# Performance work log

Measured on AMD Instinct MI355X. Metric: run time of the kernel, lower is better.

The kernel has to match this reference:

```python
import jax, jax.numpy as jnp
import numpy as np

HEADS = 8
DIM_HEAD = 64
LN_EPS = 1e-5


def rotate_half(x):
    # pairs (x0,x1) -> (-x1,x0), interleaved layout (einops '(d r)' with r=2)
    x1 = x[..., 0::2]
    x2 = x[..., 1::2]
    return jnp.stack((-x2, x1), axis=-1).reshape(x.shape)


def apply_rope(freqs, x):
    return x * jnp.cos(freqs) + rotate_half(x) * jnp.sin(freqs)


def setup_inputs() -> dict:
    key = jax.random.key(0)
    ks = jax.random.split(key, 4)
    b, n, dim = 2, 4096, 512
    inner = HEADS * DIM_HEAD
    x = jax.random.normal(ks[0], (b, n, dim), dtype=jnp.float32)
    rotary_time_emb = jax.random.uniform(ks[1], (b, n, DIM_HEAD), jnp.float32, 0.0, 6.283185)
    ln_w = jnp.ones((dim,), jnp.float32)
    ln_b = jnp.zeros((dim,), jnp.float32)
    w_qkv = jax.random.normal(ks[2], (inner * 3, dim), jnp.float32) * (dim ** -0.5)
    w_out = jax.random.normal(ks[3], (dim, inner), jnp.float32) * (inner ** -0.5)
    b_out = jnp.zeros((dim,), jnp.float32)
    return dict(x=x, rotary_time_emb=rotary_time_emb, ln_w=ln_w, ln_b=ln_b,
                w_qkv=w_qkv, w_out=w_out, b_out=b_out)


def reference(x, rotary_time_emb, ln_w, ln_b, w_qkv, w_out, b_out):
    b, n, dim = x.shape
    # LayerNorm
    mu = jnp.mean(x, axis=-1, keepdims=True)
    var = jnp.var(x, axis=-1, keepdims=True)
    xn = (x - mu) * jax.lax.rsqrt(var + LN_EPS) * ln_w + ln_b
    # QKV projection (Linear, no bias)
    qkv = xn @ w_qkv.T  # [b, n, 3*inner]
    q, k, v = jnp.split(qkv, 3, axis=-1)

    def to_heads(t):
        return t.reshape(b, n, HEADS, DIM_HEAD).transpose(0, 2, 1, 3)  # b h n d

    q, k, v = to_heads(q), to_heads(k), to_heads(v)
    freqs = rotary_time_emb[:, None, :, :]  # b 1 n d, broadcast over heads
    q = apply_rope(freqs, q)
    k = apply_rope(freqs, k)
    v = apply_rope(freqs, v)  # rotate_value=True
    scale = jnp.asarray(DIM_HEAD ** -0.5, dtype=x.dtype)
    scores = jnp.einsum('bhqd,bhkd->bhqk', q, k) * scale
    attn = jax.nn.softmax(scores, axis=-1)
    out = jnp.einsum('bhqk,bhkd->bhqd', attn, v)
    out = apply_rope(-freqs, out)  # inverse rotation of the output
    out = out.transpose(0, 2, 1, 3).reshape(b, n, HEADS * DIM_HEAD)
    return out @ w_out.T + b_out
```

## Files before the change

kernel.cpp:

```cpp
#include <hip/hip_runtime.h>
#include <cmath>

typedef short bf16x8 __attribute__((ext_vector_type(8)));
typedef float f32x2 __attribute__((ext_vector_type(2)));
typedef float f32x4 __attribute__((ext_vector_type(4)));
typedef float f32x16 __attribute__((ext_vector_type(16)));

#define NSEQ 4096
#define BATCH 2
#define DIM 512
#define HEADS 8
#define NROWS (BATCH * NSEQ)
#define QKVN (3 * DIM)

__device__ __forceinline__ unsigned short f2bf(float f) {
  unsigned int u = __float_as_uint(f);
  u += 0x7fffu + ((u >> 16) & 1u);
  return (unsigned short)(u >> 16);
}
__device__ __forceinline__ float bf2f(unsigned short h) {
  return __uint_as_float(((unsigned int)h) << 16);
}
__device__ __forceinline__ void gload16(const unsigned short* g, unsigned short* l) {
  __builtin_amdgcn_global_load_lds((const __attribute__((address_space(1))) unsigned int*)g,
                                   (__attribute__((address_space(3))) unsigned int*)l, 16, 0, 0);
}

__global__ __launch_bounds__(256) void k_tables(const float* __restrict__ rot,
                                                float* __restrict__ cosT,
                                                float* __restrict__ sinT) {
  int i = blockIdx.x * 256 + threadIdx.x;
  float f = rot[i];
  cosT[i] = cosf(f);
  sinT[i] = sinf(f);
}

__global__ __launch_bounds__(256) void k_cvt(const float* __restrict__ src,
                                             unsigned short* __restrict__ dst, int n) {
  int i = blockIdx.x * 256 + threadIdx.x;
  if (i < n) dst[i] = f2bf(src[i]);
}

__global__ __launch_bounds__(256) void k_ln(const float* __restrict__ x,
                                            const float* __restrict__ w,
                                            const float* __restrict__ bb,
                                            unsigned short* __restrict__ xn) {
  int row = blockIdx.x * 4 + (threadIdx.x >> 6);
  int lane = threadIdx.x & 63;
  const float* xr = x + (size_t)row * DIM;
  float v[8];
  float s = 0.f;
#pragma unroll
  for (int j = 0; j < 8; ++j) { v[j] = xr[lane + j * 64]; s += v[j]; }
#pragma unroll
  for (int m = 1; m < 64; m <<= 1) s += __shfl_xor(s, m);
  float mu = s * (1.0f / DIM);
  float q = 0.f;
#pragma unroll
  for (int j = 0; j < 8; ++j) { float d = v[j] - mu; q += d * d; }
#pragma unroll
  for (int m = 1; m < 64; m <<= 1) q += __shfl_xor(q, m);
  float rs = rsqrtf(q * (1.0f / DIM) + 1e-5f);
#pragma unroll
  for (int j = 0; j < 8; ++j) {
    int col = lane + j * 64;
    xn[(size_t)row * DIM + col] = f2bf((v[j] - mu) * rs * w[col] + bb[col]);
  }
}

template <int EPI>
__global__ __launch_bounds__(256) void k_gemm(const unsigned short* __restrict__ A,
                                              const unsigned short* __restrict__ B,
                                              void* __restrict__ C,
                                              const float* __restrict__ bias,
                                              int M, int N, int K) {
  __shared__ __align__(16) unsigned short As[2][128 * 32];
  __shared__ __align__(16) unsigned short Bs[2][128 * 32];
  int bm = blockIdx.x, bn = blockIdx.y;
  int tid = threadIdx.x;
  int lane = tid & 63, w = tid >> 6;
  int wm = (w >> 1) << 6, wn = (w & 1) << 6;
  f32x4 acc[4][4] = {};

#define GSTAGE(KT, BUF) do { \
  _Pragma("unroll") \
  for (int i = 0; i < 2; ++i) { \
    int c = tid + (i << 8); \
    int row = c >> 2, kc = (c & 3) << 3; \
    gload16(A + (size_t)(bm * 128 + row) * K + (KT) + kc, &As[BUF][(w * 64 + i * 256) * 8]); \
    gload16(B + (size_t)(bn * 128 + row) * K + (KT) + kc, &Bs[BUF][(w * 64 + i * 256) * 8]); \
  } } while (0)

  GSTAGE(0, 0);
  __syncthreads();
  int nk = K >> 5;
  for (int t = 0; t < nk; ++t) {
    int cur = t & 1;
    if (t + 1 < nk) GSTAGE((t + 1) << 5, cur ^ 1);
    bf16x8 af[4], bfr[4];
#pragma unroll
    for (int mi = 0; mi < 4; ++mi)
      af[mi] = *(const bf16x8*)&As[cur][(wm + mi * 16 + (lane & 15)) * 32 + ((lane >> 4) << 3)];
#pragma unroll
    for (int ni = 0; ni < 4; ++ni)
      bfr[ni] = *(const bf16x8*)&Bs[cur][(wn + ni * 16 + (lane & 15)) * 32 + ((lane >> 4) << 3)];
#pragma unroll
    for (int mi = 0; mi < 4; ++mi)
#pragma unroll
      for (int ni = 0; ni < 4; ++ni)
        acc[mi][ni] = __builtin_amdgcn_mfma_f32_16x16x32_bf16(af[mi], bfr[ni], acc[mi][ni], 0, 0, 0);
    __syncthreads();
  }
#undef GSTAGE
#pragma unroll
  for (int mi = 0; mi < 4; ++mi) {
#pragma unroll
    for (int ni = 0; ni < 4; ++ni) {
#pragma unroll
      for (int r = 0; r < 4; ++r) {
        int gm = bm * 128 + wm + mi * 16 + ((lane >> 4) << 2) + r;
        int gn = bn * 128 + wn + ni * 16 + (lane & 15);
        if (EPI == 0) {
          ((unsigned short*)C)[(size_t)gm * N + gn] = f2bf(acc[mi][ni][r]);
        } else {
          ((float*)C)[(size_t)gm * N + gn] = acc[mi][ni][r] + bias[gn];
        }
      }
    }
  }
}

__global__ __launch_bounds__(256) void k_rope_split(const unsigned short* __restrict__ qkv,
                                                    const float* __restrict__ cosT,
                                                    const float* __restrict__ sinT,
                                                    unsigned short* __restrict__ qh,
                                                    unsigned short* __restrict__ kh,
                                                    unsigned short* __restrict__ vt) {
  __shared__ unsigned short vs[128][65];
  const float QSC = 0.125f * 1.44269504f;
  int nt = blockIdx.x, bh = blockIdx.y;
  int b = bh >> 3, h = bh & 7;
  int n0 = nt * 128;
  int t = threadIdx.x;
  int sub = t >> 3, cc = t & 7;
#pragma unroll
  for (int rr = 0; rr < 4; ++rr) {
    int row = rr * 32 + sub;
    int n = n0 + row;
    size_t base = ((size_t)(b * NSEQ + n)) * QKVN + h * 64 + cc * 8;
    const float* cb = cosT + ((size_t)(b * NSEQ + n)) * 64 + cc * 8;
    const float* sb = sinT + ((size_t)(b * NSEQ + n)) * 64 + cc * 8;
    float c[8], sn[8];
#pragma unroll
    for (int j = 0; j < 8; ++j) { c[j] = cb[j]; sn[j] = sb[j]; }
    bf16x8 qv = *(const bf16x8*)(qkv + base);
    bf16x8 kv = *(const bf16x8*)(qkv + base + 512);
    bf16x8 vv = *(const bf16x8*)(qkv + base + 1024);
    union { bf16x8 v; unsigned short u[8]; } yq, yk;
#pragma unroll
    for (int j = 0; j < 8; j += 2) {
      {
        float e = bf2f((unsigned short)qv[j]), o = bf2f((unsigned short)qv[j + 1]);
        yq.u[j]     = f2bf((e * c[j] - o * sn[j]) * QSC);
        yq.u[j + 1] = f2bf((o * c[j + 1] + e * sn[j + 1]) * QSC);
      }
      {
        float e = bf2f((unsigned short)kv[j]), o = bf2f((unsigned short)kv[j + 1]);
        yk.u[j]     = f2bf(e * c[j] - o * sn[j]);
        yk.u[j + 1] = f2bf(o * c[j + 1] + e * sn[j + 1]);
      }
      {
        float e = bf2f((unsigned short)vv[j]), o = bf2f((unsigned short)vv[j + 1]);
        vs[row][cc * 8 + j]     = f2bf(e * c[j] - o * sn[j]);
        vs[row][cc * 8 + j + 1] = f2bf(o * c[j + 1] + e * sn[j + 1]);
      }
    }
    *(bf16x8*)(qh + ((size_t)bh * NSEQ + n) * 64 + cc * 8) = yq.v;
    *(bf16x8*)(kh + ((size_t)bh * NSEQ + n) * 64 + cc * 8) = yk.v;
  }
  __syncthreads();
  int d = t >> 2, c4 = t & 3;
#pragma unroll
  for (int g = 0; g < 4; ++g) {
    union { bf16x8 v; unsigned short u[8]; } tv;
#pragma unroll
    for (int j = 0; j < 8; ++j) tv.u[j] = vs[c4 * 32 + g * 8 + j][d];
    *(bf16x8*)(vt + ((size_t)bh * 64 + d) * NSEQ + n0 + c4 * 32 + g * 8) = tv.v;
  }
}

__global__ __launch_bounds__(256, 2) void k_attn(const unsigned short* __restrict__ Qh,
                                                 const unsigned short* __restrict__ Kh,
                                                 const unsigned short* __restrict__ VT,
                                                 float* __restrict__ opart,
                                                 float* __restrict__ lpart) {
  __shared__ __align__(16) unsigned short Ks[2][64 * 64];
  __shared__ __align__(16) unsigned short Vs[2][64 * 64];
  int bid = blockIdx.x;
  int bh   = (bid & 7) + 8 * ((bid >> 7) & 1);
  int qt   = (bid >> 3) & 15;
  int half = (bid >> 8) & 1;
  int tid = threadIdx.x;
  int w = tid >> 6, lane = tid & 63;
  int lq = lane & 31, hi = lane >> 5;
  int q0 = qt * 256 + w * 64;
  int kv0 = half * 2048;

  const unsigned short* Kbh = Kh + (size_t)bh * NSEQ * 64;
  const unsigned short* Vbh = VT + (size_t)bh * 64 * NSEQ;

  const unsigned short* QbA = Qh + ((size_t)bh * NSEQ + q0 + lq) * 64 + hi * 8;
  const unsigned short* QbB = QbA + 32 * 64;
  bf16x8 qfA[4], qfB[4];
#pragma unroll
  for (int j = 0; j < 4; ++j) {
    qfA[j] = *(const bf16x8*)(QbA + j * 16);
    qfB[j] = *(const bf16x8*)(QbB + j * 16);
  }

  int c0 = w * 64 + lane;
  int r0 = c0 >> 3, sw0 = ((c0 & 7) ^ (r0 & 7)) << 3;
  int c1 = c0 + 256;
  int r1 = c1 >> 3, sw1 = ((c1 & 7) ^ (r1 & 7)) << 3;
  int ld0 = (w * 64) * 8, ld1 = (256 + w * 64) * 8;

  f32x16 accA0 = (f32x16)0.0f, accA1 = (f32x16)0.0f;
  f32x16 accB0 = (f32x16)0.0f, accB1 = (f32x16)0.0f;
  float lA = 0.f, lB = 0.f;
  int swz = (lq & 7) << 4;

  gload16(Kbh + ((size_t)kv0 + r0) * 64 + sw0, &Ks[0][ld0]);
  gload16(Kbh + ((size_t)kv0 + r1) * 64 + sw1, &Ks[0][ld1]);
  gload16(Vbh + (size_t)r0 * NSEQ + kv0 + sw0, &Vs[0][ld0]);
  gload16(Vbh + (size_t)r1 * NSEQ + kv0 + sw1, &Vs[0][ld1]);
  __syncthreads();

  for (int t = 0; t < 32; ++t) {
    int cur = t & 1;
    if (t < 31) {
      int tg = kv0 + (t + 1) * 64;
      gload16(Kbh + ((size_t)tg + r0) * 64 + sw0, &Ks[cur ^ 1][ld0]);
      gload16(Kbh + ((size_t)tg + r1) * 64 + sw1, &Ks[cur ^ 1][ld1]);
      gload16(Vbh + (size_t)r0 * NSEQ + tg + sw0, &Vs[cur ^ 1][ld0]);
      gload16(Vbh + (size_t)r1 * NSEQ + tg + sw1, &Vs[cur ^ 1][ld1]);
    }
    const char* kb_ = (const char*)&Ks[cur][0];
    const char* vb_ = (const char*)&Vs[cur][0];
#pragma unroll
    for (int ph = 0; ph < 2; ++ph) {
      f32x16 sA = (f32x16)0.0f, sB = (f32x16)0.0f;
      __builtin_amdgcn_s_setprio(1);
#pragma unroll
      for (int j = 0; j < 4; ++j) {
        int cb = j * 32 + hi * 16;
        bf16x8 a = *(const bf16x8*)(kb_ + (ph * 32 + lq) * 128 + (cb ^ swz));
        sA = __builtin_amdgcn_mfma_f32_32x32x16_bf16(a, qfA[j], sA, 0, 0, 0);
        sB = __builtin_amdgcn_mfma_f32_32x32x16_bf16(a, qfB[j], sB, 0, 0, 0);
      }
      __builtin_amdgcn_s_setprio(0);
#pragma unroll
      for (int r = 0; r < 16; ++r) sA[r] = __builtin_amdgcn_exp2f(sA[r]);
#pragma unroll
      for (int r = 0; r < 16; ++r) sB[r] = __builtin_amdgcn_exp2f(sB[r]);
      {
        union { f32x16 v; f32x2 p[8]; } ua, ub; ua.v = sA; ub.v = sB;
        f32x2 a01 = ua.p[0] + ua.p[1], a23 = ua.p[2] + ua.p[3];
        f32x2 a45 = ua.p[4] + ua.p[5], a67 = ua.p[6] + ua.p[7];
        f32x2 ta = (a01 + a23) + (a45 + a67);
        lA += ta.x + ta.y;
        f32x2 b01 = ub.p[0] + ub.p[1], b23 = ub.p[2] + ub.p[3];
        f32x2 b45 = ub.p[4] + ub.p[5], b67 = ub.p[6] + ub.p[7];
        f32x2 tb = (b01 + b23) + (b45 + b67);
        lB += tb.x + tb.y;
      }
      unsigned int dwA[8], dwB[8];
#pragma unroll
      for (int m = 0; m < 8; ++m) {
        asm("v_cvt_pk_bf16_f32 %0, %1, %2" : "=v"(dwA[m]) : "v"(sA[2 * m]), "v"(sA[2 * m + 1]));
        asm("v_cvt_pk_bf16_f32 %0, %1, %2" : "=v"(dwB[m]) : "v"(sB[2 * m]), "v"(sB[2 * m + 1]));
      }
      __builtin_amdgcn_s_setprio(1);
#pragma unroll
      for (int kk = 0; kk < 2; ++kk) {
        const int B = 4 * kk;
        unsigned int svA0 = hi ? dwA[B + 0] : dwA[B + 2];
        unsigned int svA1 = hi ? dwA[B + 1] : dwA[B + 3];
        unsigned int svB0 = hi ? dwB[B + 0] : dwB[B + 2];
        unsigned int svB1 = hi ? dwB[B + 1] : dwB[B + 3];
        unsigned int rvA0 = (unsigned int)__shfl_xor((int)svA0, 32);
        unsigned int rvA1 = (unsigned int)__shfl_xor((int)svA1, 32);
        unsigned int rvB0 = (unsigned int)__shfl_xor((int)svB0, 32);
        unsigned int rvB1 = (unsigned int)__shfl_xor((int)svB1, 32);
        union { unsigned int d[4]; bf16x8 v; } puA, puB;
        puA.d[0] = hi ? rvA0 : dwA[B + 0];
        puA.d[1] = hi ? rvA1 : dwA[B + 1];
        puA.d[2] = hi ? dwA[B + 2] : rvA0;
        puA.d[3] = hi ? dwA[B + 3] : rvA1;
        puB.d[0] = hi ? rvB0 : dwB[B + 0];
        puB.d[1] = hi ? rvB1 : dwB[B + 1];
        puB.d[2] = hi ? dwB[B + 2] : rvB0;
        puB.d[3] = hi ? dwB[B + 3] : rvB1;
        int cb = (ph * 2 + kk) * 32 + hi * 16;
        bf16x8 v0 = *(const bf16x8*)(vb_ + lq * 128 + (cb ^ swz));
        bf16x8 v1 = *(const bf16x8*)(vb_ + (32 + lq) * 128 + (cb ^ swz));
        accA0 = __builtin_amdgcn_mfma_f32_32x32x16_bf16(v0, puA.v, accA0, 0, 0, 0);
        accA1 = __builtin_amdgcn_mfma_f32_32x32x16_bf16(v1, puA.v, accA1, 0, 0, 0);
        accB0 = __builtin_amdgcn_mfma_f32_32x32x16_bf16(v0, puB.v, accB0, 0, 0, 0);
        accB1 = __builtin_amdgcn_mfma_f32_32x32x16_bf16(v1, puB.v, accB1, 0, 0, 0);
      }
      __builtin_amdgcn_s_setprio(0);
    }
    __syncthreads();
  }

  float lsumA = lA + __shfl_xor(lA, 32);
  float lsumB = lB + __shfl_xor(lB, 32);
  size_t qrowA = (size_t)(half * 16 + bh) * NSEQ + q0 + lq;
  size_t qrowB = qrowA + 32;
  if (hi == 0) {
    lpart[qrowA] = lsumA;
    lpart[qrowB] = lsumB;
  }
  float* obA = opart + qrowA * 64;
  float* obB = opart + qrowB * 64;
#pragma unroll
  for (int rg = 0; rg < 4; ++rg) {
    float4 a0 = make_float4(accA0[4 * rg + 0], accA0[4 * rg + 1], accA0[4 * rg + 2], accA0[4 * rg + 3]);
    float4 a1 = make_float4(accA1[4 * rg + 0], accA1[4 * rg + 1], accA1[4 * rg + 2], accA1[4 * rg + 3]);
    float4 b0 = make_float4(accB0[4 * rg + 0], accB0[4 * rg + 1], accB0[4 * rg + 2], accB0[4 * rg + 3]);
    float4 b1 = make_float4(accB1[4 * rg + 0], accB1[4 * rg + 1], accB1[4 * rg + 2], accB1[4 * rg + 3]);
    *(float4*)(obA + 8 * rg + 4 * hi) = a0;
    *(float4*)(obA + 32 + 8 * rg + 4 * hi) = a1;
    *(float4*)(obB + 8 * rg + 4 * hi) = b0;
    *(float4*)(obB + 32 + 8 * rg + 4 * hi) = b1;
  }
}

__global__ __launch_bounds__(256) void k_combine(const float* __restrict__ opart,
                                                 const float* __restrict__ lpart,
                                                 const float* __restrict__ cosT,
                                                 const float* __restrict__ sinT,
                                                 unsigned short* __restrict__ ao) {
  int bh = blockIdx.y;
  int b = bh >> 3, h = bh & 7;
  int t = threadIdx.x;
  int q = blockIdx.x * 16 + (t >> 4);
  int d = (t & 15) * 4;
  size_t i0 = (size_t)bh * NSEQ + q;
  const size_t HOFF = (size_t)16 * NSEQ;
  float4 o0 = *(const float4*)(opart + i0 * 64 + d);
  float4 o1 = *(const float4*)(opart + (i0 + HOFF) * 64 + d);
  float inv = 1.0f / (lpart[i0] + lpart[i0 + HOFF]);
  float4 c4 = *(const float4*)(cosT + ((size_t)b * NSEQ + q) * 64 + d);
  float4 s4 = *(const float4*)(sinT + ((size_t)b * NSEQ + q) * 64 + d);
  float yx = (o0.x + o1.x) * inv;
  float yy = (o0.y + o1.y) * inv;
  float yz = (o0.z + o1.z) * inv;
  float yw = (o0.w + o1.w) * inv;
  float r0 = yx * c4.x + yy * s4.x;
  float r1 = yy * c4.y - yx * s4.y;
  float r2 = yz * c4.z + yw * s4.z;
  float r3 = yw * c4.w - yz * s4.w;
  unsigned int w0, w1;
  asm("v_cvt_pk_bf16_f32 %0, %1, %2" : "=v"(w0) : "v"(r0), "v"(r1));
  asm("v_cvt_pk_bf16_f32 %0, %1, %2" : "=v"(w1) : "v"(r2), "v"(r3));
  unsigned int uu[2] = {w0, w1};
  *(uint2*)(ao + ((size_t)b * NSEQ + q) * DIM + h * 64 + d) = *(uint2*)uu;
}

extern "C" void kernel_launch(void* const* d_in, const int* in_sizes, int n_in,
                              void* d_out, int out_size, void* d_ws, size_t ws_size,
                              hipStream_t stream) {
  const float* x    = (const float*)d_in[0];
  const float* rot  = (const float*)d_in[1];
  const float* lnw  = (const float*)d_in[2];
  const float* lnb  = (const float*)d_in[3];
  const float* wqkv = (const float*)d_in[4];
  const float* wout = (const float*)d_in[5];
  const float* bout = (const float*)d_in[6];
  float* out = (float*)d_out;

  char* ws = (char*)d_ws;
  const size_t MB = (size_t)1 << 20;
  float* cosT          = (float*)(ws + 0 * MB);
  float* sinT          = (float*)(ws + 2 * MB);
  unsigned short* wqkb = (unsigned short*)(ws + 4 * MB);
  float* lpart         = (float*)(ws + 5 * MB + 512 * 1024);
  unsigned short* wob  = (unsigned short*)(ws + 6 * MB);
  unsigned short* xn   = (unsigned short*)(ws + 8 * MB);
  float* opart         = (float*)(ws + 8 * MB);
  unsigned short* qkv  = (unsigned short*)(ws + 16 * MB);
  unsigned short* qh   = (unsigned short*)(ws + 40 * MB);
  unsigned short* ao   = (unsigned short*)(ws + 40 * MB);
  unsigned short* kh   = (unsigned short*)(ws + 48 * MB);
  unsigned short* vt   = (unsigned short*)(ws + 56 * MB);

  k_tables<<<(BATCH * NSEQ * 64) / 256, 256, 0, stream>>>(rot, cosT, sinT);
  k_cvt<<<(QKVN * DIM + 255) / 256, 256, 0, stream>>>(wqkv, wqkb, QKVN * DIM);
  k_cvt<<<(DIM * DIM + 255) / 256, 256, 0, stream>>>(wout, wob, DIM * DIM);
  k_ln<<<NROWS / 4, 256, 0, stream>>>(x, lnw, lnb, xn);
  k_gemm<0><<<dim3(NROWS / 128, QKVN / 128), 256, 0, stream>>>(xn, wqkb, qkv, nullptr,
                                                               NROWS, QKVN, DIM);
  k_rope_split<<<dim3(NSEQ / 128, 16), 256, 0, stream>>>(qkv, cosT, sinT, qh, kh, vt);
  k_attn<<<512, 256, 0, stream>>>(qh, kh, vt, opart, lpart);
  k_combine<<<dim3(NSEQ / 16, 16), 256, 0, stream>>>(opart, lpart, cosT, sinT, ao);
  k_gemm<1><<<dim3(NROWS / 128, DIM / 128), 256, 0, stream>>>(ao, wob, out, bout,
                                                              NROWS, DIM, DIM);
}
```

Baseline: 148.1 us.

## Split attention KV range into four parts and store partial outputs as bf16

Attention now splits the key/value sequence into four 1024-long chunks instead of two, doubling the grid to 1024 blocks and raising the launch-bounds occupancy hint to 4 blocks per CU. The aim is better load balance and latency hiding across the 256 CUs. Partial outputs are written as bf16 instead of fp32, so the workspace traffic stays about the same despite twice as many partials. The combine kernel sums four partials, which adds bf16 rounding error to the unnormalised accumulators. lpart moves to avoid overlapping the larger buffer.

Result: slower. 581.5 us (+292.6%).

```diff
diff --git a/kernel.cpp b/kernel.cpp
--- a/kernel.cpp
+++ b/kernel.cpp
@@ -189,22 +189,22 @@
   }
 }
 
-__global__ __launch_bounds__(256, 2) void k_attn(const unsigned short* __restrict__ Qh,
+__global__ __launch_bounds__(256, 4) void k_attn(const unsigned short* __restrict__ Qh,
                                                  const unsigned short* __restrict__ Kh,
                                                  const unsigned short* __restrict__ VT,
-                                                 float* __restrict__ opart,
+                                                 unsigned short* __restrict__ opart,
                                                  float* __restrict__ lpart) {
   __shared__ __align__(16) unsigned short Ks[2][64 * 64];
   __shared__ __align__(16) unsigned short Vs[2][64 * 64];
   int bid = blockIdx.x;
   int bh   = (bid & 7) + 8 * ((bid >> 7) & 1);
   int qt   = (bid >> 3) & 15;
-  int half = (bid >> 8) & 1;
+  int quarter = (bid >> 8) & 3;
   int tid = threadIdx.x;
   int w = tid >> 6, lane = tid & 63;
   int lq = lane & 31, hi = lane >> 5;
   int q0 = qt * 256 + w * 64;
-  int kv0 = half * 2048;
+  int kv0 = quarter << 10;
 
   const unsigned short* Kbh = Kh + (size_t)bh * NSEQ * 64;
   const unsigned short* Vbh = VT + (size_t)bh * 64 * NSEQ;
@@ -235,9 +235,9 @@
   gload16(Vbh + (size_t)r1 * NSEQ + kv0 + sw1, &Vs[0][ld1]);
   __syncthreads();
 
-  for (int t = 0; t < 32; ++t) {
+  for (int t = 0; t < 16; ++t) {
     int cur = t & 1;
-    if (t < 31) {
+    if (t < 15) {
       int tg = kv0 + (t + 1) * 64;
       gload16(Kbh + ((size_t)tg + r0) * 64 + sw0, &Ks[cur ^ 1][ld0]);
       gload16(Kbh + ((size_t)tg + r1) * 64 + sw1, &Ks[cur ^ 1][ld1]);
@@ -315,28 +315,33 @@
 
   float lsumA = lA + __shfl_xor(lA, 32);
   float lsumB = lB + __shfl_xor(lB, 32);
-  size_t qrowA = (size_t)(half * 16 + bh) * NSEQ + q0 + lq;
+  size_t qrowA = (size_t)(quarter * 16 + bh) * NSEQ + q0 + lq;
   size_t qrowB = qrowA + 32;
   if (hi == 0) {
     lpart[qrowA] = lsumA;
     lpart[qrowB] = lsumB;
   }
-  float* obA = opart + qrowA * 64;
-  float* obB = opart + qrowB * 64;
+  unsigned short* obA = opart + qrowA * 64;
+  unsigned short* obB = opart + qrowB * 64;
 #pragma unroll
   for (int rg = 0; rg < 4; ++rg) {
-    float4 a0 = make_float4(accA0[4 * rg + 0], accA0[4 * rg + 1], accA0[4 * rg + 2], accA0[4 * rg + 3]);
-    float4 a1 = make_float4(accA1[4 * rg + 0], accA1[4 * rg + 1], accA1[4 * rg + 2], accA1[4 * rg + 3]);
-    float4 b0 = make_float4(accB0[4 * rg + 0], accB0[4 * rg + 1], accB0[4 * rg + 2], accB0[4 * rg + 3]);
-    float4 b1 = make_float4(accB1[4 * rg + 0], accB1[4 * rg + 1], accB1[4 * rg + 2], accB1[4 * rg + 3]);
-    *(float4*)(obA + 8 * rg + 4 * hi) = a0;
-    *(float4*)(obA + 32 + 8 * rg + 4 * hi) = a1;
-    *(float4*)(obB + 8 * rg + 4 * hi) = b0;
-    *(float4*)(obB + 32 + 8 * rg + 4 * hi) = b1;
-  }
-}
-
-__global__ __launch_bounds__(256) void k_combine(const float* __restrict__ opart,
+    unsigned int pa0[2], pa1[2], pb0[2], pb1[2];
+    asm("v_cvt_pk_bf16_f32 %0, %1, %2" : "=v"(pa0[0]) : "v"(accA0[4 * rg + 0]), "v"(accA0[4 * rg + 1]));
+    asm("v_cvt_pk_bf16_f32 %0, %1, %2" : "=v"(pa0[1]) : "v"(accA0[4 * rg + 2]), "v"(accA0[4 * rg + 3]));
+    asm("v_cvt_pk_bf16_f32 %0, %1, %2" : "=v"(pa1[0]) : "v"(accA1[4 * rg + 0]), "v"(accA1[4 * rg + 1]));
+    asm("v_cvt_pk_bf16_f32 %0, %1, %2" : "=v"(pa1[1]) : "v"(accA1[4 * rg + 2]), "v"(accA1[4 * rg + 3]));
+    asm("v_cvt_pk_bf16_f32 %0, %1, %2" : "=v"(pb0[0]) : "v"(accB0[4 * rg + 0]), "v"(accB0[4 * rg + 1]));
+    asm("v_cvt_pk_bf16_f32 %0, %1, %2" : "=v"(pb0[1]) : "v"(accB0[4 * rg + 2]), "v"(accB0[4 * rg + 3]));
+    asm("v_cvt_pk_bf16_f32 %0, %1, %2" : "=v"(pb1[0]) : "v"(accB1[4 * rg + 0]), "v"(accB1[4 * rg + 1]));
+    asm("v_cvt_pk_bf16_f32 %0, %1, %2" : "=v"(pb1[1]) : "v"(accB1[4 * rg + 2]), "v"(accB1[4 * rg + 3]));
+    *(uint2*)(obA + 8 * rg + 4 * hi) = *(uint2*)pa0;
+    *(uint2*)(obA + 32 + 8 * rg + 4 * hi) = *(uint2*)pa1;
+    *(uint2*)(obB + 8 * rg + 4 * hi) = *(uint2*)pb0;
+    *(uint2*)(obB + 32 + 8 * rg + 4 * hi) = *(uint2*)pb1;
+  }
+}
+
+__global__ __launch_bounds__(256) void k_combine(const unsigned short* __restrict__ opart,
                                                  const float* __restrict__ lpart,
                                                  const float* __restrict__ cosT,
                                                  const float* __restrict__ sinT,
@@ -347,16 +352,25 @@
   int q = blockIdx.x * 16 + (t >> 4);
   int d = (t & 15) * 4;
   size_t i0 = (size_t)bh * NSEQ + q;
-  const size_t HOFF = (size_t)16 * NSEQ;
-  float4 o0 = *(const float4*)(opart + i0 * 64 + d);
-  float4 o1 = *(const float4*)(opart + (i0 + HOFF) * 64 + d);
-  float inv = 1.0f / (lpart[i0] + lpart[i0 + HOFF]);
+  const size_t QOFF = (size_t)16 * NSEQ;
+  float l = lpart[i0] + lpart[i0 + QOFF] + lpart[i0 + 2 * QOFF] + lpart[i0 + 3 * QOFF];
+  float o[4] = {0.f, 0.f, 0.f, 0.f};
+#pragma unroll
+  for (int p = 0; p < 4; ++p) {
+    uint2 u = *(const uint2*)(opart + (i0 + p * QOFF) * 64 + d);
+    unsigned int u0 = u.x, u1 = u.y;
+    o[0] += bf2f((unsigned short)(u0 & 0xffff));
+    o[1] += bf2f((unsigned short)(u0 >> 16));
+    o[2] += bf2f((unsigned short)(u1 & 0xffff));
+    o[3] += bf2f((unsigned short)(u1 >> 16));
+  }
+  float inv = 1.0f / l;
   float4 c4 = *(const float4*)(cosT + ((size_t)b * NSEQ + q) * 64 + d);
   float4 s4 = *(const float4*)(sinT + ((size_t)b * NSEQ + q) * 64 + d);
-  float yx = (o0.x + o1.x) * inv;
-  float yy = (o0.y + o1.y) * inv;
-  float yz = (o0.z + o1.z) * inv;
-  float yw = (o0.w + o1.w) * inv;
+  float yx = o[0] * inv;
+  float yy = o[1] * inv;
+  float yz = o[2] * inv;
+  float yw = o[3] * inv;
   float r0 = yx * c4.x + yy * s4.x;
   float r1 = yy * c4.y - yx * s4.y;
   float r2 = yz * c4.z + yw * s4.z;
@@ -385,10 +399,10 @@
   float* cosT          = (float*)(ws + 0 * MB);
   float* sinT          = (float*)(ws + 2 * MB);
   unsigned short* wqkb = (unsigned short*)(ws + 4 * MB);
-  float* lpart         = (float*)(ws + 5 * MB + 512 * 1024);
   unsigned short* wob  = (unsigned short*)(ws + 6 * MB);
+  float* lpart         = (float*)(ws + 6 * MB + 512 * 1024);
   unsigned short* xn   = (unsigned short*)(ws + 8 * MB);
-  float* opart         = (float*)(ws + 8 * MB);
+  unsigned short* opart = (unsigned short*)(ws + 8 * MB);
   unsigned short* qkv  = (unsigned short*)(ws + 16 * MB);
   unsigned short* qh   = (unsigned short*)(ws + 40 * MB);
   unsigned short* ao   = (unsigned short*)(ws + 40 * MB);
@@ -402,7 +416,7 @@
   k_gemm<0><<<dim3(NROWS / 128, QKVN / 128), 256, 0, stream>>>(xn, wqkb, qkv, nullptr,
                                                                NROWS, QKVN, DIM);
   k_rope_split<<<dim3(NSEQ / 128, 16), 256, 0, stream>>>(qkv, cosT, sinT, qh, kh, vt);
-  k_attn<<<512, 256, 0, stream>>>(qh, kh, vt, opart, lpart);
+  k_attn<<<1024, 256, 0, stream>>>(qh, kh, vt, opart, lpart);
   k_combine<<<dim3(NSEQ / 16, 16), 256, 0, stream>>>(opart, lpart, cosT, sinT, ao);
   k_gemm<1><<<dim3(NROWS / 128, DIM / 128), 256, 0, stream>>>(ao, wob, out, bout,
                                                               NROWS, DIM, DIM);
```

## Deepen K/V prefetch pipeline to four LDS buffers with explicit vmcnt waits

Applied to the files above, without the earlier changes.

The attention kernel's K/V shared-memory ring grows from two to four buffers, with loads issued two tiles ahead. Each iteration now waits on s_waitcnt vmcnt and a single barrier instead of two __syncthreads, to hide global-load latency. LDS use doubles to 64 KB per block, which may limit occupancy at the two-blocks-per-CU launch bound. Correctness depends on the manual vmcnt counts matching the loads in flight and on four buffers being enough to avoid overwriting a tile still being read.

Measured after the change: 147.4 us. Within noise of the previous version (-0.5%).

```diff
diff --git a/kernel.cpp b/kernel.cpp
--- a/kernel.cpp
+++ b/kernel.cpp
@@ -194,8 +194,8 @@
                                                  const unsigned short* __restrict__ VT,
                                                  float* __restrict__ opart,
                                                  float* __restrict__ lpart) {
-  __shared__ __align__(16) unsigned short Ks[2][64 * 64];
-  __shared__ __align__(16) unsigned short Vs[2][64 * 64];
+  __shared__ __align__(16) unsigned short Ks[4][64 * 64];
+  __shared__ __align__(16) unsigned short Vs[4][64 * 64];
   int bid = blockIdx.x;
   int bh   = (bid & 7) + 8 * ((bid >> 7) & 1);
   int qt   = (bid >> 3) & 15;
@@ -229,23 +229,31 @@
   float lA = 0.f, lB = 0.f;
   int swz = (lq & 7) << 4;
 
-  gload16(Kbh + ((size_t)kv0 + r0) * 64 + sw0, &Ks[0][ld0]);
-  gload16(Kbh + ((size_t)kv0 + r1) * 64 + sw1, &Ks[0][ld1]);
-  gload16(Vbh + (size_t)r0 * NSEQ + kv0 + sw0, &Vs[0][ld0]);
-  gload16(Vbh + (size_t)r1 * NSEQ + kv0 + sw1, &Vs[0][ld1]);
-  __syncthreads();
+#define STAGE(T, BUF) do { \
+  int tg_ = kv0 + (T) * 64; \
+  gload16(Kbh + ((size_t)tg_ + r0) * 64 + sw0, &Ks[BUF][ld0]); \
+  gload16(Kbh + ((size_t)tg_ + r1) * 64 + sw1, &Ks[BUF][ld1]); \
+  gload16(Vbh + (size_t)r0 * NSEQ + tg_ + sw0, &Vs[BUF][ld0]); \
+  gload16(Vbh + (size_t)r1 * NSEQ + tg_ + sw1, &Vs[BUF][ld1]); \
+} while (0)
+
+  STAGE(0, 0);
+  STAGE(1, 1);
 
   for (int t = 0; t < 32; ++t) {
-    int cur = t & 1;
-    if (t < 31) {
-      int tg = kv0 + (t + 1) * 64;
-      gload16(Kbh + ((size_t)tg + r0) * 64 + sw0, &Ks[cur ^ 1][ld0]);
-      gload16(Kbh + ((size_t)tg + r1) * 64 + sw1, &Ks[cur ^ 1][ld1]);
-      gload16(Vbh + (size_t)r0 * NSEQ + tg + sw0, &Vs[cur ^ 1][ld0]);
-      gload16(Vbh + (size_t)r1 * NSEQ + tg + sw1, &Vs[cur ^ 1][ld1]);
+    int rd = t & 3;
+    if (t < 30) {
+      STAGE(t + 2, (t + 2) & 3);
+      asm volatile("s_waitcnt vmcnt(8)" ::: "memory");
+    } else if (t == 30) {
+      asm volatile("s_waitcnt vmcnt(4)" ::: "memory");
+    } else {
+      asm volatile("s_waitcnt vmcnt(0)" ::: "memory");
     }
-    const char* kb_ = (const char*)&Ks[cur][0];
-    const char* vb_ = (const char*)&Vs[cur][0];
+    __builtin_amdgcn_s_barrier();
+    asm volatile("" ::: "memory");
+    const char* kb_ = (const char*)&Ks[rd][0];
+    const char* vb_ = (const char*)&Vs[rd][0];
 #pragma unroll
     for (int ph = 0; ph < 2; ++ph) {
       f32x16 sA = (f32x16)0.0f, sB = (f32x16)0.0f;
@@ -310,8 +318,8 @@
       }
       __builtin_amdgcn_s_setprio(0);
     }
-    __syncthreads();
-  }
+  }
+#undef STAGE
 
   float lsumA = lA + __shfl_xor(lA, 32);
   float lsumB = lB + __shfl_xor(lB, 32);
```
